# Kernel tuning notes

Hardware: AMD Instinct MI355X
Metric: run time of the kernel (lower is better)

Reference implementation:

```python
import jax, jax.numpy as jnp
import numpy as np

N_ACTIVE = 200000
N_IN = 64
N_OUT = 64
K = 27          # filter volume (3^3)
R = 100000      # rulebook pairs per filter offset


def setup_inputs() -> dict:
    key = jax.random.key(0)
    k1, k2, k3, k4 = jax.random.split(key, 4)
    std = (2.0 / (N_IN * K)) ** 0.5
    features = jax.random.normal(k1, (N_ACTIVE, N_IN), dtype=jnp.float32)
    weight = jax.random.normal(k2, (N_IN * K, N_OUT), dtype=jnp.float32) * std
    bias = jnp.zeros((N_OUT,), dtype=jnp.float32)
    in_idx = jax.random.randint(k3, (K, R), 0, N_ACTIVE, dtype=jnp.int64 if jax.config.jax_enable_x64 else jnp.int32)
    out_idx = jax.random.randint(k4, (K, R), 0, N_ACTIVE, dtype=jnp.int64 if jax.config.jax_enable_x64 else jnp.int32)
    return {"features": features, "weight": weight, "bias": bias,
            "in_idx": in_idx, "out_idx": out_idx}


def reference(features, weight, bias, in_idx, out_idx):
    # Rulebook-based submanifold sparse convolution:
    # for each filter offset k: gather inputs, matmul with weight slice,
    # scatter-accumulate into output sites. Bias added once per active site.
    n_active, n_in = features.shape
    k = in_idx.shape[0]
    W = weight.reshape(k, n_in, -1)            # [K, nIn, nOut]
    gathered = features[in_idx]                # [K, R, nIn]  (irregular gather)
    contrib = jnp.einsum('kri,kio->kro', gathered, W)  # grouped matmul
    out = jnp.zeros((n_active, W.shape[2]), dtype=features.dtype)
    out = out.at[out_idx.reshape(-1)].add(contrib.reshape(-1, W.shape[2]))
    return out + bias
```

## Files before the change

kernel.cpp:

```cpp
#include <hip/hip_runtime.h>
#include <stdint.h>

#define N_ACTIVE 200000
#define N_IN 64
#define N_OUT 64
#define K_FILT 27
#define R_PAIRS 100000
#define TOTP (K_FILT * R_PAIRS)
#define NSLOT (N_ACTIVE * K_FILT)

#define CF_BLOCKS (N_ACTIVE * N_IN / 8 / 256)
#define CW_BLOCKS K_FILT
#define CL_BLOCKS ((TOTP + 255) / 256)

typedef __bf16 bf16x8 __attribute__((ext_vector_type(8)));
typedef float f32x4 __attribute__((ext_vector_type(4)));

__global__ __launch_bounds__(256) void prep_fused(
    const float* __restrict__ feat, __bf16* __restrict__ featb,
    const float* __restrict__ wsrc, __bf16* __restrict__ wt,
    const int* __restrict__ in_idx, const int* __restrict__ out_idx,
    int* __restrict__ slotCnt,
    int* __restrict__ slot1, int* __restrict__ slot2, int* __restrict__ slot3,
    int2* __restrict__ ovf, int* __restrict__ ovfCur)
{
    int bb = blockIdx.x, t = threadIdx.x;
    if (bb < CF_BLOCKS) {
        int i = bb * 256 + t;
        const f32x4* src = reinterpret_cast<const f32x4*>(feat) + 2 * (size_t)i;
        f32x4 v0 = __builtin_nontemporal_load(src);
        f32x4 v1 = __builtin_nontemporal_load(src + 1);
        bf16x8 o;
        o[0] = (__bf16)v0[0]; o[1] = (__bf16)v0[1]; o[2] = (__bf16)v0[2]; o[3] = (__bf16)v0[3];
        o[4] = (__bf16)v1[0]; o[5] = (__bf16)v1[1]; o[6] = (__bf16)v1[2]; o[7] = (__bf16)v1[3];
        reinterpret_cast<bf16x8*>(featb)[i] = o;
    } else if (bb < CF_BLOCKS + CW_BLOCKS) {
        int kf = bb - CF_BLOCKS;
        const float* wk = wsrc + kf * 4096;
        __bf16* wo = wt + kf * 4096;
        int o = t >> 2, i0 = (t & 3) * 16;
        bf16x8 a, b;
        #pragma unroll
        for (int j = 0; j < 8; ++j) a[j] = (__bf16)wk[(i0 + j) * 64 + o];
        #pragma unroll
        for (int j = 0; j < 8; ++j) b[j] = (__bf16)wk[(i0 + 8 + j) * 64 + o];
        *reinterpret_cast<bf16x8*>(wo + o * 64 + i0) = a;
        *reinterpret_cast<bf16x8*>(wo + o * 64 + i0 + 8) = b;
    } else {
        int p = (bb - CF_BLOCKS - CW_BLOCKS) * 256 + t;
        if (p < TOTP) {
            unsigned k = (unsigned)p / (unsigned)R_PAIRS;
            int row = __builtin_nontemporal_load(&out_idx[p]);
            int iv  = __builtin_nontemporal_load(&in_idx[p]);
            int slot = row * K_FILT + (int)k;
            int c = atomicAdd(&slotCnt[slot], 1);
            if (c == 0)      slot1[slot] = iv;
            else if (c == 1) slot2[slot] = iv;
            else if (c == 2) slot3[slot] = iv;
            else {
                int q = atomicAdd(ovfCur, 1);
                ovf[q] = make_int2(slot, iv);
            }
        }
    }
}

__global__ __launch_bounds__(256, 3) void conv_slots(
    const __bf16* __restrict__ featb,
    const __bf16* __restrict__ wtb,
    const float* __restrict__ bias,
    const int* __restrict__ slotCnt,
    const int* __restrict__ slot1, const int* __restrict__ slot2,
    const int* __restrict__ slot3,
    float* __restrict__ out)
{
    const int t = threadIdx.x;
    const int w = t >> 6;
    const int lane = t & 63;
    const int lrow = lane & 15;
    const int kg   = lane >> 4;
    const int kgo  = kg * 8;
    const int rowBase = blockIdx.x * 64 + w * 16;
    const int slotBase = (rowBase + lrow) * K_FILT;

    f32x4 acc0 = {0.f,0.f,0.f,0.f}, acc1 = acc0, acc2 = acc0, acc3 = acc0;
    const float b0 = bias[lrow], b1 = bias[16 + lrow],
                b2 = bias[32 + lrow], b3 = bias[48 + lrow];
    const bf16x8 zero8 = {};

    #pragma unroll 3
    for (int kf = 0; kf < K_FILT; ++kf) {
        const int slot = slotBase + kf;
        int c  = __builtin_nontemporal_load(&slotCnt[slot]);
        int s1 = __builtin_nontemporal_load(&slot1[slot]);
        int s2 = __builtin_nontemporal_load(&slot2[slot]);
        int s3 = __builtin_nontemporal_load(&slot3[slot]);
        int a1 = (c > 0) ? s1 : 0;
        int a2 = (c > 1) ? s2 : 0;
        int a3 = (c > 2) ? s3 : 0;

        const __bf16* p1 = featb + (size_t)a1 * 64 + kgo;
        const __bf16* p2 = featb + (size_t)a2 * 64 + kgo;
        const __bf16* p3 = featb + (size_t)a3 * 64 + kgo;
        bf16x8 x0 = *reinterpret_cast<const bf16x8*>(p1);
        bf16x8 x1 = *reinterpret_cast<const bf16x8*>(p1 + 32);
        bf16x8 y0 = *reinterpret_cast<const bf16x8*>(p2);
        bf16x8 y1 = *reinterpret_cast<const bf16x8*>(p2 + 32);
        bf16x8 z0 = *reinterpret_cast<const bf16x8*>(p3);
        bf16x8 z1 = *reinterpret_cast<const bf16x8*>(p3 + 32);

        const __bf16* wk = wtb + kf * 4096;
        bf16x8 bf00 = *reinterpret_cast<const bf16x8*>(wk + (lrow)      * 64 + kgo);
        bf16x8 bf01 = *reinterpret_cast<const bf16x8*>(wk + (lrow)      * 64 + 32 + kgo);
        bf16x8 bf10 = *reinterpret_cast<const bf16x8*>(wk + (16 + lrow) * 64 + kgo);
        bf16x8 bf11 = *reinterpret_cast<const bf16x8*>(wk + (16 + lrow) * 64 + 32 + kgo);
        bf16x8 bf20 = *reinterpret_cast<const bf16x8*>(wk + (32 + lrow) * 64 + kgo);
        bf16x8 bf21 = *reinterpret_cast<const bf16x8*>(wk + (32 + lrow) * 64 + 32 + kgo);
        bf16x8 bf30 = *reinterpret_cast<const bf16x8*>(wk + (48 + lrow) * 64 + kgo);
        bf16x8 bf31 = *reinterpret_cast<const bf16x8*>(wk + (48 + lrow) * 64 + 32 + kgo);

        x0 = (c > 0) ? x0 : zero8;  x1 = (c > 0) ? x1 : zero8;
        y0 = (c > 1) ? y0 : zero8;  y1 = (c > 1) ? y1 : zero8;
        z0 = (c > 2) ? z0 : zero8;  z1 = (c > 2) ? z1 : zero8;
        bf16x8 A0, A1;
        #pragma unroll
        for (int j = 0; j < 8; ++j) {
            float f0 = (float)x0[j] + (float)y0[j] + (float)z0[j];
            float f1 = (float)x1[j] + (float)y1[j] + (float)z1[j];
            A0[j] = (__bf16)f0;
            A1[j] = (__bf16)f1;
        }

        acc0 = __builtin_amdgcn_mfma_f32_16x16x32_bf16(A0, bf00, acc0, 0, 0, 0);
        acc0 = __builtin_amdgcn_mfma_f32_16x16x32_bf16(A1, bf01, acc0, 0, 0, 0);
        acc1 = __builtin_amdgcn_mfma_f32_16x16x32_bf16(A0, bf10, acc1, 0, 0, 0);
        acc1 = __builtin_amdgcn_mfma_f32_16x16x32_bf16(A1, bf11, acc1, 0, 0, 0);
        acc2 = __builtin_amdgcn_mfma_f32_16x16x32_bf16(A0, bf20, acc2, 0, 0, 0);
        acc2 = __builtin_amdgcn_mfma_f32_16x16x32_bf16(A1, bf21, acc2, 0, 0, 0);
        acc3 = __builtin_amdgcn_mfma_f32_16x16x32_bf16(A0, bf30, acc3, 0, 0, 0);
        acc3 = __builtin_amdgcn_mfma_f32_16x16x32_bf16(A1, bf31, acc3, 0, 0, 0);
    }

    #pragma unroll
    for (int r = 0; r < 4; ++r) {
        int gr = rowBase + kg * 4 + r;
        float* orow = out + (size_t)gr * 64;
        __builtin_nontemporal_store(acc0[r] + b0, &orow[lrow]);
        __builtin_nontemporal_store(acc1[r] + b1, &orow[16 + lrow]);
        __builtin_nontemporal_store(acc2[r] + b2, &orow[32 + lrow]);
        __builtin_nontemporal_store(acc3[r] + b3, &orow[48 + lrow]);
    }
}

__global__ __launch_bounds__(64) void ovf_cleanup(
    const __bf16* __restrict__ featb, const __bf16* __restrict__ wtb,
    const int2* __restrict__ ovf, const int* __restrict__ ovfCur,
    float* __restrict__ out)
{
    const int n = *ovfCur;
    const int lane = threadIdx.x;
    for (int e = blockIdx.x; e < n; e += gridDim.x) {
        int2 v = ovf[e];
        int slot = v.x, in = v.y;
        int row = slot / K_FILT;
        int kf  = slot - row * K_FILT;
        const __bf16* fp = featb + (size_t)in * 64;
        const __bf16* wp = wtb + kf * 4096 + lane * 64;
        float s = 0.f;
        #pragma unroll
        for (int j = 0; j < 8; ++j) {
            bf16x8 fv = *reinterpret_cast<const bf16x8*>(fp + j * 8);
            bf16x8 wv = *reinterpret_cast<const bf16x8*>(wp + j * 8);
            #pragma unroll
            for (int q = 0; q < 8; ++q) s += (float)fv[q] * (float)wv[q];
        }
        atomicAdd(&out[(size_t)row * 64 + lane], s);
    }
}

extern "C" void kernel_launch(void* const* d_in, const int* in_sizes, int n_in,
                              void* d_out, int out_size, void* d_ws, size_t ws_size,
                              hipStream_t stream) {
    const float* feat    = (const float*)d_in[0];
    const float* weight  = (const float*)d_in[1];
    const float* bias    = (const float*)d_in[2];
    const int*   in_idx  = (const int*)d_in[3];
    const int*   out_idx = (const int*)d_in[4];
    float* out = (float*)d_out;

    char* wsb = (char*)d_ws;
    __bf16* featb  = (__bf16*)wsb;
    __bf16* wtb    = (__bf16*)(wsb + 25600000);
    int*  slotCnt  = (int*) (wsb + 25600000 + 221184);
    int*  slot1    = slotCnt + NSLOT;
    int*  slot2    = slot1 + NSLOT;
    int*  slot3    = slot2 + NSLOT;
    int*  ovfCur   = slot3 + NSLOT;
    int2* ovf      = (int2*)(ovfCur + 4);

    hipMemsetAsync(slotCnt, 0, (size_t)NSLOT * 4, stream);
    hipMemsetAsync(ovfCur, 0, 16, stream);

    prep_fused<<<dim3(CF_BLOCKS + CW_BLOCKS + CL_BLOCKS), dim3(256), 0, stream>>>(
        feat, featb, weight, wtb, in_idx, out_idx,
        slotCnt, slot1, slot2, slot3, ovf, ovfCur);
    conv_slots<<<dim3(N_ACTIVE / 64), dim3(256), 0, stream>>>(
        featb, wtb, bias, slotCnt, slot1, slot2, slot3, out);
    ovf_cleanup<<<dim3(2048), dim3(64), 0, stream>>>(featb, wtb, ovf, ovfCur, out);
}
```

Before: 664.5 us.

## Interleave slot count and indices into int4 records, raise occupancy and unroll

Replaces the four separate slot arrays (count plus three index arrays) with one interleaved int4 record per slot. The prep kernel's atomic and its index writes now land in the same cache line, and the conv kernel reads each slot with a single 16-byte load instead of four scattered ones. It also raises the launch-bounds occupancy hint from 3 to 4, lifts the kf-loop unroll from 3 to 9, and drops the nontemporal hints on the rulebook loads. The memset now covers four times as many bytes, and the higher occupancy target may force register spills.

```diff
diff --git a/kernel.cpp b/kernel.cpp
--- a/kernel.cpp
+++ b/kernel.cpp
@@ -20,8 +20,7 @@
     const float* __restrict__ feat, __bf16* __restrict__ featb,
     const float* __restrict__ wsrc, __bf16* __restrict__ wt,
     const int* __restrict__ in_idx, const int* __restrict__ out_idx,
-    int* __restrict__ slotCnt,
-    int* __restrict__ slot1, int* __restrict__ slot2, int* __restrict__ slot3,
+    int* __restrict__ slotW,
     int2* __restrict__ ovf, int* __restrict__ ovfCur)
 {
     int bb = blockIdx.x, t = threadIdx.x;
@@ -50,13 +49,11 @@
         int p = (bb - CF_BLOCKS - CW_BLOCKS) * 256 + t;
         if (p < TOTP) {
             unsigned k = (unsigned)p / (unsigned)R_PAIRS;
-            int row = __builtin_nontemporal_load(&out_idx[p]);
-            int iv  = __builtin_nontemporal_load(&in_idx[p]);
+            int row = out_idx[p];
+            int iv  = in_idx[p];
             int slot = row * K_FILT + (int)k;
-            int c = atomicAdd(&slotCnt[slot], 1);
-            if (c == 0)      slot1[slot] = iv;
-            else if (c == 1) slot2[slot] = iv;
-            else if (c == 2) slot3[slot] = iv;
+            int c = atomicAdd(&slotW[slot * 4], 1);
+            if (c < 3) slotW[slot * 4 + 1 + c] = iv;
             else {
                 int q = atomicAdd(ovfCur, 1);
                 ovf[q] = make_int2(slot, iv);
@@ -65,13 +62,11 @@
     }
 }
 
-__global__ __launch_bounds__(256, 3) void conv_slots(
+__global__ __launch_bounds__(256, 4) void conv_slots(
     const __bf16* __restrict__ featb,
     const __bf16* __restrict__ wtb,
     const float* __restrict__ bias,
-    const int* __restrict__ slotCnt,
-    const int* __restrict__ slot1, const int* __restrict__ slot2,
-    const int* __restrict__ slot3,
+    const int4* __restrict__ slotT,
     float* __restrict__ out)
 {
     const int t = threadIdx.x;
@@ -88,16 +83,13 @@
                 b2 = bias[32 + lrow], b3 = bias[48 + lrow];
     const bf16x8 zero8 = {};
 
-    #pragma unroll 3
+    #pragma unroll 9
     for (int kf = 0; kf < K_FILT; ++kf) {
-        const int slot = slotBase + kf;
-        int c  = __builtin_nontemporal_load(&slotCnt[slot]);
-        int s1 = __builtin_nontemporal_load(&slot1[slot]);
-        int s2 = __builtin_nontemporal_load(&slot2[slot]);
-        int s3 = __builtin_nontemporal_load(&slot3[slot]);
-        int a1 = (c > 0) ? s1 : 0;
-        int a2 = (c > 1) ? s2 : 0;
-        int a3 = (c > 2) ? s3 : 0;
+        int4 sv = slotT[slotBase + kf];
+        int c  = sv.x;
+        int a1 = (c > 0) ? sv.y : 0;
+        int a2 = (c > 1) ? sv.z : 0;
+        int a3 = (c > 2) ? sv.w : 0;
 
         const __bf16* p1 = featb + (size_t)a1 * 64 + kgo;
         const __bf16* p2 = featb + (size_t)a2 * 64 + kgo;
@@ -191,20 +183,16 @@
     char* wsb = (char*)d_ws;
     __bf16* featb  = (__bf16*)wsb;
     __bf16* wtb    = (__bf16*)(wsb + 25600000);
-    int*  slotCnt  = (int*) (wsb + 25600000 + 221184);
-    int*  slot1    = slotCnt + NSLOT;
-    int*  slot2    = slot1 + NSLOT;
-    int*  slot3    = slot2 + NSLOT;
-    int*  ovfCur   = slot3 + NSLOT;
+    int*  slotW    = (int*) (wsb + 25600000 + 221184);
+    int*  ovfCur   = slotW + (size_t)NSLOT * 4;
     int2* ovf      = (int2*)(ovfCur + 4);
 
-    hipMemsetAsync(slotCnt, 0, (size_t)NSLOT * 4, stream);
+    hipMemsetAsync(slotW, 0, (size_t)NSLOT * 16, stream);
     hipMemsetAsync(ovfCur, 0, 16, stream);
 
     prep_fused<<<dim3(CF_BLOCKS + CW_BLOCKS + CL_BLOCKS), dim3(256), 0, stream>>>(
-        feat, featb, weight, wtb, in_idx, out_idx,
-        slotCnt, slot1, slot2, slot3, ovf, ovfCur);
+        feat, featb, weight, wtb, in_idx, out_idx, slotW, ovf, ovfCur);
     conv_slots<<<dim3(N_ACTIVE / 64), dim3(256), 0, stream>>>(
-        featb, wtb, bias, slotCnt, slot1, slot2, slot3, out);
+        featb, wtb, bias, (const int4*)slotW, out);
     ovf_cleanup<<<dim3(2048), dim3(64), 0, stream>>>(featb, wtb, ovf, ovfCur, out);
 }
```

After: 627.1 us. -5.6%, faster.
